# Performance work log

Measured on AMD Instinct MI355X. Metric: run time of the kernel, lower is better.

Reference implementation:

```python
import jax, jax.numpy as jnp
import numpy as np

B, S, D = 1, 4096, 1024
H, G = 16, 4
DK = D // H            # 64, per-head dim
HKV = H // G           # 4 KV heads
DKV = D // G           # 256, KV projection width
SCALE = 1.0 / np.sqrt(np.float32(DK))


def setup_inputs() -> dict:
    key = jax.random.key(0)
    ks = jax.random.split(key, 10)
    std = 0.02
    return {
        "x": jax.random.normal(ks[0], (B, S, D), jnp.float32),
        "mask": jax.random.bernoulli(ks[1], 0.1, (B, 1, S)),  # True = masked out
        "Wq": jax.random.normal(ks[2], (D, D), jnp.float32) * std,
        "bq": jnp.zeros((D,), jnp.float32),
        "Wk": jax.random.normal(ks[3], (D, DKV), jnp.float32) * std,
        "bk": jnp.zeros((DKV,), jnp.float32),
        "Wv": jax.random.normal(ks[4], (D, DKV), jnp.float32) * std,
        "bv": jnp.zeros((DKV,), jnp.float32),
        "Wo": jax.random.normal(ks[5], (D, D), jnp.float32) * std,
        "bo": jnp.zeros((D,), jnp.float32),
    }


def reference(x, mask, Wq, bq, Wk, bk, Wv, bv, Wo, bo):
    b, s, _ = x.shape
    # projections
    q = (x @ Wq + bq).reshape(b, s, H, DK).transpose(0, 2, 1, 3)      # [B,H,S,DK]
    k = (x @ Wk + bk).reshape(b, s, HKV, DK).transpose(0, 2, 1, 3)    # [B,HKV,S,DK]
    v = (x @ Wv + bv).reshape(b, s, HKV, DK).transpose(0, 2, 1, 3)    # [B,HKV,S,DK]
    # expand KV heads: head h = kv_head * G + g (matches torch expand+reshape)
    k = jnp.repeat(k, G, axis=1)                                       # [B,H,S,DK]
    v = jnp.repeat(v, G, axis=1)                                       # [B,H,S,DK]
    scores = jnp.einsum("bhsd,bhtd->bhst", q, k) * SCALE              # [B,H,S,S]
    neg_inf = jnp.finfo(scores.dtype).min
    scores = jnp.where(mask[:, None, :, :], neg_inf, scores)           # mask: [B,1,1,S]
    attn = jax.nn.softmax(scores, axis=-1)
    out = jnp.einsum("bhst,bhtd->bhsd", attn, v)                      # [B,H,S,DK]
    out = out.transpose(0, 2, 1, 3).reshape(b, s, D)
    return out @ Wo + bo
```

## Files before the change

### kernel.cpp

```cpp
#include <hip/hip_runtime.h>
#include <cstdint>
#include <cstddef>

#define S_LEN 4096
#define DMODEL 1024
#define NHEADS 16
#define HDK 64
#define DKV 256
#define NTOT 1536
#define QSCALE 0.18033688011112042f

typedef __bf16 bf16;
typedef __bf16 bf16x8 __attribute__((ext_vector_type(8)));
typedef float f32x4 __attribute__((ext_vector_type(4)));

typedef __attribute__((address_space(3))) void lds_void;
typedef const __attribute__((address_space(1))) void gbl_void;

__device__ __forceinline__ void gload16(const void* g, void* l) {
  __builtin_amdgcn_global_load_lds((gbl_void*)g, (lds_void*)l, 16, 0, 0);
}

__global__ __launch_bounds__(256) void prep(
    const float* __restrict__ x, const int* __restrict__ mask,
    const float* __restrict__ Wq, const float* __restrict__ Wk,
    const float* __restrict__ Wv, const float* __restrict__ Wo,
    bf16* __restrict__ xb, float* __restrict__ mkf, bf16* __restrict__ mkb,
    bf16* __restrict__ Wqt, bf16* __restrict__ Wkt,
    bf16* __restrict__ Wvt, bf16* __restrict__ Wot) {
  const int z = blockIdx.z;
  if (z < 4) {
    const float* src;
    bf16* dst;
    int C;
    switch (z) {
      case 0: src = Wq; dst = Wqt; C = DMODEL; break;
      case 1: src = Wk; dst = Wkt; C = DKV; break;
      case 2: src = Wv; dst = Wvt; C = DKV; break;
      default: src = Wo; dst = Wot; C = DMODEL; break;
    }
    const int c0 = blockIdx.x * 32;
    if (c0 >= C) return;
    __shared__ float tile[32][33];
    const int tx = threadIdx.x & 31;
    const int ty = threadIdx.x >> 5;
    const int r0 = blockIdx.y * 32;
#pragma unroll
    for (int i = 0; i < 4; i++)
      tile[ty + i * 8][tx] = src[(size_t)(r0 + ty + i * 8) * C + c0 + tx];
    __syncthreads();
#pragma unroll
    for (int i = 0; i < 4; i++)
      dst[(size_t)(c0 + ty + i * 8) * DMODEL + r0 + tx] = (bf16)tile[tx][ty + i * 8];
  } else {
    const int b = blockIdx.y * 32 + blockIdx.x;
    const int half = z - 4;
    const int i = ((half * 1024 + b) * 256 + (int)threadIdx.x) * 8;
    float4 a = *(const float4*)(x + i);
    float4 c = *(const float4*)(x + i + 4);
    bf16 o[8] = {(bf16)a.x, (bf16)a.y, (bf16)a.z, (bf16)a.w,
                 (bf16)c.x, (bf16)c.y, (bf16)c.z, (bf16)c.w};
    *(uint4*)(xb + i) = *(uint4*)o;
    if (half == 1 && b < 2) {
      const int mi = (b * 256 + (int)threadIdx.x) * 8;
#pragma unroll
      for (int j = 0; j < 8; j++) {
        float keep = mask[mi + j] ? 0.0f : 1.0f;
        mkf[mi + j] = keep;
        mkb[mi + j] = (bf16)keep;
      }
    }
  }
}

template <int QKV>
__global__ __launch_bounds__(256) void gemm_ld(
    const bf16* __restrict__ A, const bf16* __restrict__ Bt, int M, int N, int K,
    int NT,
    const float* __restrict__ bq, const float* __restrict__ bk,
    const float* __restrict__ bv, const float* __restrict__ mkf,
    bf16* __restrict__ Qb, bf16* __restrict__ Kb, bf16* __restrict__ Vtb,
    const float* __restrict__ bo, float* __restrict__ Co) {
  __shared__ bf16 As[64 * 64];
  __shared__ bf16 Bs[128 * 64];
  const int t = threadIdx.x;
  const int lane = t & 63;
  const int wave = t >> 6;

  const int bid = blockIdx.x;
  const int xcd = bid & 7;
  const int local = bid >> 3;
  const int m_local = local / NT;
  const int ntile = local - m_local * NT;
  const int mchunk = (M >> 6) >> 3;
  const int m0 = (xcd * mchunk + m_local) * 64;
  const int n0 = ntile * 128;

  const int wm = (wave >> 1) * 32;
  const int wn = (wave & 1) * 64;
  const int lr = lane & 15;
  const int quad = lane >> 4;

  const int sr = lane >> 3;
  const int sc = ((lane & 7) ^ (lane >> 3)) * 8;

  f32x4 acc[2][4] = {};

  for (int k0 = 0; k0 < K; k0 += 64) {
    __syncthreads();
#pragma unroll
    for (int j = 0; j < 2; j++) {
      const int rbase = wave * 16 + j * 8;
      gload16(A + (size_t)(m0 + rbase + sr) * K + k0 + sc, &As[rbase * 64]);
    }
#pragma unroll
    for (int j = 0; j < 4; j++) {
      const int rbase = wave * 32 + j * 8;
      gload16(Bt + (size_t)(n0 + rbase + sr) * K + k0 + sc, &Bs[rbase * 64]);
    }
    __syncthreads();
#pragma unroll
    for (int kh2 = 0; kh2 < 2; kh2++) {
      const int fo = ((kh2 * 4 + quad) ^ (lr & 7)) * 8;
      bf16x8 af[2], bfr[4];
#pragma unroll
      for (int mt = 0; mt < 2; mt++)
        af[mt] = *(const bf16x8*)(&As[(wm + mt * 16 + lr) * 64 + fo]);
#pragma unroll
      for (int nt = 0; nt < 4; nt++)
        bfr[nt] = *(const bf16x8*)(&Bs[(wn + nt * 16 + lr) * 64 + fo]);
#pragma unroll
      for (int mt = 0; mt < 2; mt++)
#pragma unroll
        for (int nt = 0; nt < 4; nt++)
          acc[mt][nt] = __builtin_amdgcn_mfma_f32_16x16x32_bf16(af[mt], bfr[nt], acc[mt][nt], 0, 0, 0);
    }
  }

#pragma unroll
  for (int nt = 0; nt < 4; nt++) {
    const int n = n0 + wn + nt * 16 + lr;
    if (QKV) {
      if (n < DMODEL) {
        const float b = bq[n];
#pragma unroll
        for (int mt = 0; mt < 2; mt++)
#pragma unroll
          for (int r = 0; r < 4; r++) {
            const int m = m0 + wm + mt * 16 + quad * 4 + r;
            Qb[(size_t)m * DMODEL + n] = (bf16)((acc[mt][nt][r] + b) * QSCALE);
          }
      } else if (n < DMODEL + DKV) {
        const float b = bk[n - DMODEL];
#pragma unroll
        for (int mt = 0; mt < 2; mt++)
#pragma unroll
          for (int r = 0; r < 4; r++) {
            const int m = m0 + wm + mt * 16 + quad * 4 + r;
            Kb[(size_t)m * DKV + (n - DMODEL)] = (bf16)(acc[mt][nt][r] + b);
          }
      } else {
        const float b = bv[n - DMODEL - DKV];
#pragma unroll
        for (int mt = 0; mt < 2; mt++)
#pragma unroll
          for (int r = 0; r < 4; r++) {
            const int m = m0 + wm + mt * 16 + quad * 4 + r;
            Vtb[(size_t)(n - DMODEL - DKV) * S_LEN + m] = (bf16)((acc[mt][nt][r] + b) * mkf[m]);
          }
      }
    } else {
      const float b = bo[n];
#pragma unroll
      for (int mt = 0; mt < 2; mt++)
#pragma unroll
        for (int r = 0; r < 4; r++) {
          const int m = m0 + wm + mt * 16 + quad * 4 + r;
          Co[(size_t)m * N + n] = acc[mt][nt][r] + b;
        }
    }
  }
}

__global__ __launch_bounds__(256) void flash_attn(
    const bf16* __restrict__ Q, const bf16* __restrict__ K,
    const bf16* __restrict__ Vt, const bf16* __restrict__ mkb,
    bf16* __restrict__ O) {
  const int h = blockIdx.y;
  const int kvh = h >> 2;
  const int q0 = blockIdx.x * 128;
  const int t = threadIdx.x;
  const int lane = t & 63;
  const int wave = t >> 6;
  const int lr = lane & 15;
  const int quad = lane >> 4;

  __shared__ bf16 Ks[2][128 * 64];
  __shared__ bf16 Vs[2][64 * 128];
  __shared__ bf16 Ps[4][32][36];

  bf16x8 aq[2][2];
#pragma unroll
  for (int qt = 0; qt < 2; qt++) {
    const int qrow = q0 + wave * 32 + qt * 16 + lr;
    aq[qt][0] = *(const bf16x8*)(Q + (size_t)qrow * DMODEL + h * HDK + quad * 8);
    aq[qt][1] = *(const bf16x8*)(Q + (size_t)qrow * DMODEL + h * HDK + 32 + quad * 8);
  }

  const bf16* Kg = K + kvh * HDK;
  const bf16* Vg = Vt + (size_t)kvh * HDK * S_LEN;
  const int krl = lane >> 3;
  const int kgc = ((lane & 7) ^ (lane >> 3)) * 8;
  const int vrl = lane >> 4;

#pragma unroll
  for (int j = 0; j < 4; j++) {
    const int rb = wave * 32 + j * 8;
    gload16(Kg + (size_t)(rb + krl) * DKV + kgc, &Ks[0][rb * 64]);
  }
#pragma unroll
  for (int j = 0; j < 4; j++) {
    const int rb = wave * 16 + j * 4;
    const int g = ((lane & 15) ^ (j * 4 + vrl)) * 8;
    gload16(Vg + (size_t)(rb + vrl) * S_LEN + g, &Vs[0][rb * 128]);
  }

  f32x4 o_acc[2][4] = {};
  f32x4 l_acc[2] = {};
  int buf = 0;

  for (int kv0 = 0; kv0 < S_LEN; kv0 += 128) {
    __syncthreads();
    const int kvn = kv0 + 128;
    if (kvn < S_LEN) {
      const int nb = buf ^ 1;
#pragma unroll
      for (int j = 0; j < 4; j++) {
        const int rb = wave * 32 + j * 8;
        gload16(Kg + (size_t)(kvn + rb + krl) * DKV + kgc, &Ks[nb][rb * 64]);
      }
#pragma unroll
      for (int j = 0; j < 4; j++) {
        const int rb = wave * 16 + j * 4;
        const int g = ((lane & 15) ^ (j * 4 + vrl)) * 8;
        gload16(Vg + (size_t)(rb + vrl) * S_LEN + kvn + g, &Vs[nb][rb * 128]);
      }
    }
    const bf16* Ksb = Ks[buf];
    const bf16* Vsb = Vs[buf];

#pragma unroll
    for (int kc = 0; kc < 4; kc++) {
      bf16x8 ak[2][2];
#pragma unroll
      for (int ntl = 0; ntl < 2; ntl++) {
        const int krow = kc * 32 + ntl * 16 + lr;
        ak[ntl][0] = *(const bf16x8*)(&Ksb[krow * 64 + ((quad) ^ (lr & 7)) * 8]);
        ak[ntl][1] = *(const bf16x8*)(&Ksb[krow * 64 + ((4 + quad) ^ (lr & 7)) * 8]);
      }
#pragma unroll
      for (int qt = 0; qt < 2; qt++) {
#pragma unroll
        for (int ntl = 0; ntl < 2; ntl++) {
          f32x4 s = {};
          s = __builtin_amdgcn_mfma_f32_16x16x32_bf16(ak[ntl][0], aq[qt][0], s, 0, 0, 0);
          s = __builtin_amdgcn_mfma_f32_16x16x32_bf16(ak[ntl][1], aq[qt][1], s, 0, 0, 0);
          bf16 p4[4];
#pragma unroll
          for (int r = 0; r < 4; r++) p4[r] = (bf16)__builtin_amdgcn_exp2f(s[r]);
          *(uint2*)(&Ps[wave][qt * 16 + lr][ntl * 16 + quad * 4]) = *(uint2*)p4;
        }
      }
      bf16x8 bvf[4];
#pragma unroll
      for (int ntv = 0; ntv < 4; ntv++) {
        const int vrow = ntv * 16 + lr;
        bvf[ntv] = *(const bf16x8*)(&Vsb[vrow * 128 + ((kc * 4 + quad) ^ lr) * 8]);
      }
      const bf16x8 mkfv = *(const bf16x8*)(mkb + kv0 + kc * 32 + quad * 8);
#pragma unroll
      for (int qt = 0; qt < 2; qt++) {
        bf16x8 ap = *(const bf16x8*)(&Ps[wave][qt * 16 + lr][quad * 8]);
#pragma unroll
        for (int ntv = 0; ntv < 4; ntv++)
          o_acc[qt][ntv] = __builtin_amdgcn_mfma_f32_16x16x32_bf16(ap, bvf[ntv], o_acc[qt][ntv], 0, 0, 0);
        l_acc[qt] = __builtin_amdgcn_mfma_f32_16x16x32_bf16(ap, mkfv, l_acc[qt], 0, 0, 0);
      }
    }
    buf ^= 1;
  }

#pragma unroll
  for (int qt = 0; qt < 2; qt++) {
#pragma unroll
    for (int ntv = 0; ntv < 4; ntv++) {
#pragma unroll
      for (int r = 0; r < 4; r++) {
        const int row = q0 + wave * 32 + qt * 16 + quad * 4 + r;
        O[(size_t)row * DMODEL + h * HDK + ntv * 16 + lr] =
            (bf16)(o_acc[qt][ntv][r] / l_acc[qt][r]);
      }
    }
  }
}

extern "C" void kernel_launch(void* const* d_in, const int* in_sizes, int n_in,
                              void* d_out, int out_size, void* d_ws, size_t ws_size,
                              hipStream_t stream) {
  const float* x = (const float*)d_in[0];
  const int* mask = (const int*)d_in[1];
  const float* Wq = (const float*)d_in[2];
  const float* bq = (const float*)d_in[3];
  const float* Wk = (const float*)d_in[4];
  const float* bk = (const float*)d_in[5];
  const float* Wv = (const float*)d_in[6];
  const float* bv = (const float*)d_in[7];
  const float* Wo = (const float*)d_in[8];
  const float* bo = (const float*)d_in[9];
  float* out = (float*)d_out;

  char* w = (char*)d_ws;
  bf16* xb  = (bf16*)w; w += (size_t)S_LEN * DMODEL * 2;
  bf16* Wqt = (bf16*)w; w += (size_t)DMODEL * DMODEL * 2;
  bf16* Wkt = (bf16*)w; w += (size_t)DKV * DMODEL * 2;
  bf16* Wvt = (bf16*)w; w += (size_t)DKV * DMODEL * 2;
  bf16* Wot = (bf16*)w; w += (size_t)DMODEL * DMODEL * 2;
  bf16* Qb  = (bf16*)w; w += (size_t)S_LEN * DMODEL * 2;
  bf16* Kb  = (bf16*)w; w += (size_t)S_LEN * DKV * 2;
  bf16* Vtb = (bf16*)w; w += (size_t)DKV * S_LEN * 2;
  bf16* Ob  = (bf16*)w; w += (size_t)S_LEN * DMODEL * 2;
  float* mkf = (float*)w; w += (size_t)S_LEN * 4;
  bf16* mkb = (bf16*)w; w += (size_t)S_LEN * 2;

  prep<<<dim3(32, 32, 6), 256, 0, stream>>>(
      x, mask, Wq, Wk, Wv, Wo, xb, mkf, mkb, Wqt, Wkt, Wvt, Wot);

  gemm_ld<1><<<dim3((S_LEN / 64) * (NTOT / 128)), 256, 0, stream>>>(
      xb, Wqt, S_LEN, NTOT, DMODEL, NTOT / 128, bq, bk, bv, mkf, Qb, Kb, Vtb,
      nullptr, nullptr);

  flash_attn<<<dim3(S_LEN / 128, NHEADS), 256, 0, stream>>>(Qb, Kb, Vtb, mkb, Ob);

  gemm_ld<0><<<dim3((S_LEN / 64) * (DMODEL / 128)), 256, 0, stream>>>(
      Ob, Wot, S_LEN, DMODEL, DMODEL, DMODEL / 128, nullptr, nullptr, nullptr,
      nullptr, nullptr, nullptr, nullptr, bo, out);
}
```

Baseline: 211.6 us.

## Switch flash attention to 32x32x16 MFMA with register-resident P via permlane32_swap

Rewrites the attention inner loop to use 32x32x16 bf16 MFMAs computing transposed scores (keys x queries). Exponentiated probabilities are packed in registers and rearranged with permlane32_swap to feed the PV MFMA directly, removing the per-wave LDS round trip for P. The output becomes O^T in accumulators, stored as 4-element vectors per lane, and s_setprio is raised around MFMA bursts. This removes LDS writes, reads and the associated waits, and uses fewer, larger MFMA instructions. In exchange it depends on exact lane layouts of the 32x32 MFMA and on the permlane swap mapping, and the larger accumulators raise register pressure.

```diff
diff --git a/kernel.cpp b/kernel.cpp
--- a/kernel.cpp
+++ b/kernel.cpp
@@ -13,6 +13,10 @@
 typedef __bf16 bf16;
 typedef __bf16 bf16x8 __attribute__((ext_vector_type(8)));
 typedef float f32x4 __attribute__((ext_vector_type(4)));
+typedef float f32x16 __attribute__((ext_vector_type(16)));
+typedef unsigned u32x2 __attribute__((ext_vector_type(2)));
+typedef unsigned u32x4 __attribute__((ext_vector_type(4)));
+typedef unsigned short u16x4 __attribute__((ext_vector_type(4)));
 
 typedef __attribute__((address_space(3))) void lds_void;
 typedef const __attribute__((address_space(1))) void gbl_void;
@@ -192,19 +196,18 @@
   const int t = threadIdx.x;
   const int lane = t & 63;
   const int wave = t >> 6;
-  const int lr = lane & 15;
-  const int quad = lane >> 4;
+  const int l31 = lane & 31;
+  const int hi = lane >> 5;
 
   __shared__ bf16 Ks[2][128 * 64];
   __shared__ bf16 Vs[2][64 * 128];
-  __shared__ bf16 Ps[4][32][36];
-
-  bf16x8 aq[2][2];
-#pragma unroll
-  for (int qt = 0; qt < 2; qt++) {
-    const int qrow = q0 + wave * 32 + qt * 16 + lr;
-    aq[qt][0] = *(const bf16x8*)(Q + (size_t)qrow * DMODEL + h * HDK + quad * 8);
-    aq[qt][1] = *(const bf16x8*)(Q + (size_t)qrow * DMODEL + h * HDK + 32 + quad * 8);
+
+  const int qrow = q0 + wave * 32 + l31;
+  bf16x8 aq[4];
+  {
+    const bf16* qp = Q + (size_t)qrow * DMODEL + h * HDK + hi * 8;
+#pragma unroll
+    for (int s = 0; s < 4; s++) aq[s] = *(const bf16x8*)(qp + s * 16);
   }
 
   const bf16* Kg = K + kvh * HDK;
@@ -225,8 +228,8 @@
     gload16(Vg + (size_t)(rb + vrl) * S_LEN + g, &Vs[0][rb * 128]);
   }
 
-  f32x4 o_acc[2][4] = {};
-  f32x4 l_acc[2] = {};
+  f32x16 o_acc[2] = {};
+  f32x16 l_acc = {};
   int buf = 0;
 
   for (int kv0 = 0; kv0 < S_LEN; kv0 += 128) {
@@ -250,56 +253,65 @@
     const bf16* Vsb = Vs[buf];
 
 #pragma unroll
-    for (int kc = 0; kc < 4; kc++) {
-      bf16x8 ak[2][2];
-#pragma unroll
-      for (int ntl = 0; ntl < 2; ntl++) {
-        const int krow = kc * 32 + ntl * 16 + lr;
-        ak[ntl][0] = *(const bf16x8*)(&Ksb[krow * 64 + ((quad) ^ (lr & 7)) * 8]);
-        ak[ntl][1] = *(const bf16x8*)(&Ksb[krow * 64 + ((4 + quad) ^ (lr & 7)) * 8]);
-      }
-#pragma unroll
-      for (int qt = 0; qt < 2; qt++) {
-#pragma unroll
-        for (int ntl = 0; ntl < 2; ntl++) {
-          f32x4 s = {};
-          s = __builtin_amdgcn_mfma_f32_16x16x32_bf16(ak[ntl][0], aq[qt][0], s, 0, 0, 0);
-          s = __builtin_amdgcn_mfma_f32_16x16x32_bf16(ak[ntl][1], aq[qt][1], s, 0, 0, 0);
-          bf16 p4[4];
-#pragma unroll
-          for (int r = 0; r < 4; r++) p4[r] = (bf16)__builtin_amdgcn_exp2f(s[r]);
-          *(uint2*)(&Ps[wave][qt * 16 + lr][ntl * 16 + quad * 4]) = *(uint2*)p4;
-        }
-      }
-      bf16x8 bvf[4];
-#pragma unroll
-      for (int ntv = 0; ntv < 4; ntv++) {
-        const int vrow = ntv * 16 + lr;
-        bvf[ntv] = *(const bf16x8*)(&Vsb[vrow * 128 + ((kc * 4 + quad) ^ lr) * 8]);
-      }
-      const bf16x8 mkfv = *(const bf16x8*)(mkb + kv0 + kc * 32 + quad * 8);
-#pragma unroll
-      for (int qt = 0; qt < 2; qt++) {
-        bf16x8 ap = *(const bf16x8*)(&Ps[wave][qt * 16 + lr][quad * 8]);
-#pragma unroll
-        for (int ntv = 0; ntv < 4; ntv++)
-          o_acc[qt][ntv] = __builtin_amdgcn_mfma_f32_16x16x32_bf16(ap, bvf[ntv], o_acc[qt][ntv], 0, 0, 0);
-        l_acc[qt] = __builtin_amdgcn_mfma_f32_16x16x32_bf16(ap, mkfv, l_acc[qt], 0, 0, 0);
-      }
+    for (int t4 = 0; t4 < 4; t4++) {
+      const int key = t4 * 32 + l31;
+      bf16x8 akf[4];
+#pragma unroll
+      for (int s = 0; s < 4; s++)
+        akf[s] = *(const bf16x8*)(&Ksb[key * 64 + ((s * 2 + hi) ^ (key & 7)) * 8]);
+      f32x16 sa = {};
+      __builtin_amdgcn_s_setprio(1);
+#pragma unroll
+      for (int s = 0; s < 4; s++)
+        sa = __builtin_amdgcn_mfma_f32_32x32x16_bf16(akf[s], aq[s], sa, 0, 0, 0);
+      __builtin_amdgcn_s_setprio(0);
+
+      unsigned pw[8];
+#pragma unroll
+      for (int i = 0; i < 8; i++) {
+        const bf16 e0 = (bf16)__builtin_amdgcn_exp2f(sa[2 * i]);
+        const bf16 e1 = (bf16)__builtin_amdgcn_exp2f(sa[2 * i + 1]);
+        pw[i] = ((unsigned)__builtin_bit_cast(unsigned short, e1) << 16) |
+                (unsigned)__builtin_bit_cast(unsigned short, e0);
+      }
+      const u32x2 s02 = __builtin_amdgcn_permlane32_swap(pw[0], pw[2], false, false);
+      const u32x2 s13 = __builtin_amdgcn_permlane32_swap(pw[1], pw[3], false, false);
+      const u32x2 s46 = __builtin_amdgcn_permlane32_swap(pw[4], pw[6], false, false);
+      const u32x2 s57 = __builtin_amdgcn_permlane32_swap(pw[5], pw[7], false, false);
+      const u32x4 b0v = {s02[0], s13[0], s02[1], s13[1]};
+      const u32x4 b1v = {s46[0], s57[0], s46[1], s57[1]};
+      const bf16x8 bp0 = __builtin_bit_cast(bf16x8, b0v);
+      const bf16x8 bp1 = __builtin_bit_cast(bf16x8, b1v);
+
+      const bf16x8 amk0 = *(const bf16x8*)(mkb + kv0 + t4 * 32 + hi * 8);
+      const bf16x8 amk1 = *(const bf16x8*)(mkb + kv0 + t4 * 32 + 16 + hi * 8);
+      __builtin_amdgcn_s_setprio(1);
+#pragma unroll
+      for (int dt = 0; dt < 2; dt++) {
+        const int d = dt * 32 + l31;
+        const bf16x8 av0 = *(const bf16x8*)(&Vsb[d * 128 + ((t4 * 4 + hi) ^ (d & 15)) * 8]);
+        const bf16x8 av1 = *(const bf16x8*)(&Vsb[d * 128 + ((t4 * 4 + 2 + hi) ^ (d & 15)) * 8]);
+        o_acc[dt] = __builtin_amdgcn_mfma_f32_32x32x16_bf16(av0, bp0, o_acc[dt], 0, 0, 0);
+        o_acc[dt] = __builtin_amdgcn_mfma_f32_32x32x16_bf16(av1, bp1, o_acc[dt], 0, 0, 0);
+      }
+      l_acc = __builtin_amdgcn_mfma_f32_32x32x16_bf16(amk0, bp0, l_acc, 0, 0, 0);
+      l_acc = __builtin_amdgcn_mfma_f32_32x32x16_bf16(amk1, bp1, l_acc, 0, 0, 0);
+      __builtin_amdgcn_s_setprio(0);
     }
     buf ^= 1;
   }
 
-#pragma unroll
-  for (int qt = 0; qt < 2; qt++) {
-#pragma unroll
-    for (int ntv = 0; ntv < 4; ntv++) {
-#pragma unroll
-      for (int r = 0; r < 4; r++) {
-        const int row = q0 + wave * 32 + qt * 16 + quad * 4 + r;
-        O[(size_t)row * DMODEL + h * HDK + ntv * 16 + lr] =
-            (bf16)(o_acc[qt][ntv][r] / l_acc[qt][r]);
-      }
+  const float linv = 1.0f / l_acc[0];
+  bf16* Orow = O + (size_t)qrow * DMODEL + h * HDK;
+#pragma unroll
+  for (int dt = 0; dt < 2; dt++) {
+#pragma unroll
+    for (int g = 0; g < 4; g++) {
+      u16x4 o4;
+#pragma unroll
+      for (int j = 0; j < 4; j++)
+        o4[j] = __builtin_bit_cast(unsigned short, (bf16)(o_acc[dt][g * 4 + j] * linv));
+      *(u16x4*)(Orow + dt * 32 + g * 8 + hi * 4) = o4;
     }
   }
 }
```

Result: slower. 222.4 us (+5.1%).

## Double-buffer LDS tiles in projection GEMM to overlap loads with MFMA

Applied to the files above, without the earlier changes.

Each GEMM block now keeps two LDS buffers for the A and B tiles. It prefetches the next K-slice with global_load_lds while running MFMAs on the current slice, and needs only one barrier per iteration instead of two. This is meant to hide global-load latency in the QKV and output projections. The cost is twice the LDS per block, which may lower occupancy, and correctness depends on the barrier also draining the outstanding async loads.

```diff
diff --git a/kernel.cpp b/kernel.cpp
--- a/kernel.cpp
+++ b/kernel.cpp
@@ -81,8 +81,8 @@
     const float* __restrict__ bv, const float* __restrict__ mkf,
     bf16* __restrict__ Qb, bf16* __restrict__ Kb, bf16* __restrict__ Vtb,
     const float* __restrict__ bo, float* __restrict__ Co) {
-  __shared__ bf16 As[64 * 64];
-  __shared__ bf16 Bs[128 * 64];
+  __shared__ bf16 As[2][64 * 64];
+  __shared__ bf16 Bs[2][128 * 64];
   const int t = threadIdx.x;
   const int lane = t & 63;
   const int wave = t >> 6;
@@ -102,39 +102,57 @@
   const int quad = lane >> 4;
 
   const int sr = lane >> 3;
-  const int sc = ((lane & 7) ^ (lane >> 3)) * 8;
+  const int sc = ((lane & 7) ^ sr) * 8;
 
   f32x4 acc[2][4] = {};
 
+#pragma unroll
+  for (int j = 0; j < 2; j++) {
+    const int rbase = wave * 16 + j * 8;
+    gload16(A + (size_t)(m0 + rbase + sr) * K + sc, &As[0][rbase * 64]);
+  }
+#pragma unroll
+  for (int j = 0; j < 4; j++) {
+    const int rbase = wave * 32 + j * 8;
+    gload16(Bt + (size_t)(n0 + rbase + sr) * K + sc, &Bs[0][rbase * 64]);
+  }
+
+  int buf = 0;
   for (int k0 = 0; k0 < K; k0 += 64) {
     __syncthreads();
-#pragma unroll
-    for (int j = 0; j < 2; j++) {
-      const int rbase = wave * 16 + j * 8;
-      gload16(A + (size_t)(m0 + rbase + sr) * K + k0 + sc, &As[rbase * 64]);
-    }
-#pragma unroll
-    for (int j = 0; j < 4; j++) {
-      const int rbase = wave * 32 + j * 8;
-      gload16(Bt + (size_t)(n0 + rbase + sr) * K + k0 + sc, &Bs[rbase * 64]);
-    }
-    __syncthreads();
+    const int kn = k0 + 64;
+    if (kn < K) {
+      const int nb = buf ^ 1;
+#pragma unroll
+      for (int j = 0; j < 2; j++) {
+        const int rbase = wave * 16 + j * 8;
+        gload16(A + (size_t)(m0 + rbase + sr) * K + kn + sc, &As[nb][rbase * 64]);
+      }
+#pragma unroll
+      for (int j = 0; j < 4; j++) {
+        const int rbase = wave * 32 + j * 8;
+        gload16(Bt + (size_t)(n0 + rbase + sr) * K + kn + sc, &Bs[nb][rbase * 64]);
+      }
+    }
+    const bf16* Asb = As[buf];
+    const bf16* Bsb = Bs[buf];
 #pragma unroll
     for (int kh2 = 0; kh2 < 2; kh2++) {
       const int fo = ((kh2 * 4 + quad) ^ (lr & 7)) * 8;
       bf16x8 af[2], bfr[4];
 #pragma unroll
       for (int mt = 0; mt < 2; mt++)
-        af[mt] = *(const bf16x8*)(&As[(wm + mt * 16 + lr) * 64 + fo]);
+        af[mt] = *(const bf16x8*)(&Asb[(wm + mt * 16 + lr) * 64 + fo]);
 #pragma unroll
       for (int nt = 0; nt < 4; nt++)
-        bfr[nt] = *(const bf16x8*)(&Bs[(wn + nt * 16 + lr) * 64 + fo]);
+        bfr[nt] = *(const bf16x8*)(&Bsb[(wn + nt * 16 + lr) * 64 + fo]);
 #pragma unroll
       for (int mt = 0; mt < 2; mt++)
 #pragma unroll
         for (int nt = 0; nt < 4; nt++)
           acc[mt][nt] = __builtin_amdgcn_mfma_f32_16x16x32_bf16(af[mt], bfr[nt], acc[mt][nt], 0, 0, 0);
     }
+    buf ^= 1;
   }
 
 #pragma unroll
```

Result: no change. 214.8 us (+1.5%).
